# Performance work log

Hardware: AMD Instinct MI355X
Metric: run time of the kernel (lower is better)

The kernel has to match this reference:

```python
import jax, jax.numpy as jnp
import numpy as np

H, W, WIN = 16, 6, 3  # tile height/width, SSIM window
C1, C2 = 0.01 ** 2, 0.03 ** 2  # kornia ssim constants (max_val=1.0)


def _gauss_kernel3():
    # kornia get_gaussian_kernel2d((3,3),(1.5,1.5)), normalized
    c = jnp.arange(WIN, dtype=jnp.float32) - (WIN - 1) / 2.0
    g = jnp.exp(-(c ** 2) / (2.0 * 1.5 ** 2))
    g = g / g.sum()
    k2 = jnp.outer(g, g)
    return (k2 / k2.sum()).reshape(-1)  # (9,)


def _patches3(x):
    # x: (N,H,W) -> (N,H,W,9) 3x3 reflect-padded neighborhoods (kornia filter2d border 'reflect')
    xp = jnp.pad(x, ((0, 0), (1, 1), (1, 1)), mode='reflect')
    rows = [xp[:, i:i + H, j:j + W] for i in range(WIN) for j in range(WIN)]
    return jnp.stack(rows, axis=-1)


def setup_inputs() -> dict:
    key = jax.random.key(0)
    k1, k2 = jax.random.split(key)
    img_tensor = jax.random.uniform(k1, (1, 1, 1024, 768), dtype=jnp.float32)
    chars = jax.random.uniform(k2, (95, 1, 16, 6), dtype=jnp.float32)
    return {"img_tensor": img_tensor, "chars": chars}


def reference(img_tensor, chars):
    img_h, img_w = img_tensor.shape[-2], img_tensor.shape[-1]
    n_rows, n_cols = img_h // H, img_w // W
    # nn.Unfold(kernel=(H,W), stride=(H,W)): row-major tiles, each flattened (h,w)
    tiles = img_tensor[0, 0].reshape(n_rows, H, n_cols, W).transpose(0, 2, 1, 3)
    tiles = tiles.reshape(-1, H, W)              # (nt,H,W)
    refs = chars[:, 0]                           # (nr,H,W)

    kflat = _gauss_kernel3()                     # (9,)
    Tp = _patches3(tiles)                        # (nt,H,W,9)
    Rp = _patches3(refs)                         # (nr,H,W,9)

    # per-image windowed stats (computed ONCE per tile / per ref)
    mu_t = Tp @ kflat                            # (nt,H,W)
    mu_r = Rp @ kflat                            # (nr,H,W)
    ex2_t = (Tp ** 2) @ kflat
    ex2_r = (Rp ** 2) @ kflat
    sig_t = ex2_t - mu_t ** 2
    sig_r = ex2_r - mu_r ** 2

    # pairwise cross term E[t*r]: contract kernel over the 3x3 window axis
    exr = jnp.einsum('thwk,rhwk->trhw', Tp * kflat, Rp)  # (nt,nr,H,W)

    mt = mu_t[:, None]                           # (nt,1,H,W)
    mr = mu_r[None, :]                           # (1,nr,H,W)
    sig_tr = exr - mt * mr
    num = (2.0 * mt * mr + C1) * (2.0 * sig_tr + C2)
    den = (mt ** 2 + mr ** 2 + C1) * (sig_t[:, None] + sig_r[None, :] + C2)
    scores = (num / den).mean(axis=(2, 3))       # (nt,nr)

    dens_t = tiles.mean(axis=(1, 2))             # (nt,)
    dens_r = refs.mean(axis=(1, 2))              # (nr,)
    scores = scores - 3.0 * jnp.abs(dens_t[:, None] - dens_r[None, :])

    best_indices = jnp.argmax(scores, axis=1)
    return best_indices.reshape(-1, n_cols)
```

## Files before the change

### kernel.cpp

```cpp
#include <hip/hip_runtime.h>
#include <math.h>


static constexpr float kC1 = 1.0e-4f;
static constexpr float kC2 = 9.0e-4f;

struct KF { float k[9]; };

__device__ __forceinline__ int refl(int x, int n) {
  if (x < 0) return -x;
  if (x >= n) return 2 * n - 2 - x;
  return x;
}

__global__ __launch_bounds__(128) void refprep_kernel(
    const float* __restrict__ chars, float* __restrict__ refdata,
    float* __restrict__ densR, KF kf) {
  const int hw = blockIdx.x;
  const int r = threadIdx.x;
  if (r >= 96) return;
  const int rp = r / 6 + 16 * (r % 6);
  float* row = refdata + ((size_t)hw * 96 + rp) * 12;
  const int h = hw / 6, w = hw % 6;
  if (r < 95) {
    const float* cb = chars + r * 96;
    float mu = 0.f, ex2 = 0.f;
    float wrv[9];
#pragma unroll
    for (int i = 0; i < 3; ++i) {
      const int hh = refl(h + i - 1, 16);
#pragma unroll
      for (int j = 0; j < 3; ++j) {
        const int ww = refl(w + j - 1, 6);
        const float p = cb[hh * 6 + ww];
        const float kv = kf.k[i * 3 + j];
        wrv[i * 3 + j] = 2.0f * kv * p;
        mu += kv * p;
        ex2 += kv * p * p;
      }
    }
    const float sig = ex2 - mu * mu;
#pragma unroll
    for (int k = 0; k < 9; ++k) row[k] = wrv[k];
    row[9]  = 2.0f * mu;
    row[10] = mu * mu + kC1;
    row[11] = sig + kC2;
  } else {
#pragma unroll
    for (int k = 0; k < 9; ++k) row[k] = 0.f;
    row[9]  = 0.f;
    row[10] = kC1;
    row[11] = kC2;
  }
  if (hw == 0) {
    if (r < 95) {
      float s = 0.f;
      for (int i = 0; i < 96; ++i) s += chars[r * 96 + i];
      densR[r] = s * (1.0f / 96.0f);
    } else {
      densR[r] = 0.f;
    }
  }
}

__device__ __forceinline__ void stage_px(const float* __restrict__ src,
                                         float* dst, int lane) {
  const uintptr_t gs = (uintptr_t)src;
  const uintptr_t ls = (uintptr_t)dst;
#define G_(off) ((const __attribute__((address_space(1))) void*)(gs + (off)))
#define L_(off) ((__attribute__((address_space(3))) void*)(uint32_t)(ls + (off)))
  __builtin_amdgcn_global_load_lds(G_(0    + lane * 16), L_(0),    16, 0, 0);
  __builtin_amdgcn_global_load_lds(G_(1024 + lane * 16), L_(1024), 16, 0, 0);
  __builtin_amdgcn_global_load_lds(G_(2048 + lane * 16), L_(2048), 16, 0, 0);
  __builtin_amdgcn_global_load_lds(G_(3072 + lane * 16), L_(3072), 16, 0, 0);
  __builtin_amdgcn_global_load_lds(G_(4096 + lane * 4),  L_(4096), 4, 0, 0);
  __builtin_amdgcn_global_load_lds(G_(4352 + lane * 4),  L_(4352), 4, 0, 0);
#undef G_
#undef L_
}

__global__ __launch_bounds__(512, 2)
void ssim_main_kernel(
    const float* __restrict__ img, const float* __restrict__ refdata,
    const float* __restrict__ densR, int* __restrict__ out, KF kf) {
  __shared__ float smem[29184];
  __shared__ float densT[32];
  float* padT = smem;
  float* statT = smem + 4608;

  const int tid = threadIdx.x;
  const int w = tid >> 6;
  const int lane = tid & 63;
  const int tthr = lane >> 4;
  const int rthr = lane & 15;
  const int tl0 = tthr * 8;
  const int blk = blockIdx.x;
  const int row0 = blk >> 2;
  const int c0 = (blk & 3) * 32;
  const int hwBase = w * 12;
  float* rbuf = smem + 10752 + w * 2304;

  stage_px(refdata + (size_t)hwBase * 1152, rbuf, lane);

  for (int idx = tid; idx < 4608; idx += 512) {
    const int c = idx >> 5, tl = idx & 31;
    const int ph = c >> 3, pw = c & 7;
    const int h = refl(ph - 1, 16), ww = refl(pw - 1, 6);
    padT[idx] = img[(row0 * 16 + h) * 768 + (c0 + tl) * 6 + ww];
  }
  __syncthreads();

  if (tid < 32) {
    float s = 0.f;
    for (int h = 0; h < 16; ++h)
      for (int ww = 0; ww < 6; ++ww)
        s += padT[((h + 1) * 8 + (ww + 1)) * 32 + tid];
    densT[tid] = s * (1.0f / 96.0f);
  }
  for (int idx = tid; idx < 3072; idx += 512) {
    const int hw = idx >> 5, tl = idx & 31;
    const int h = hw / 6, ww = hw % 6;
    float mu = 0.f, ex2 = 0.f;
#pragma unroll
    for (int i = 0; i < 3; ++i)
#pragma unroll
      for (int j = 0; j < 3; ++j) {
        const float p = padT[((h + i) * 8 + (ww + j)) * 32 + tl];
        const float kv = kf.k[i * 3 + j];
        mu += kv * p;
        ex2 += kv * p * p;
      }
    statT[idx] = mu;
    statT[3072 + idx] = ex2 - mu * mu;
  }
  __syncthreads();

  float score[8][6];
#pragma unroll
  for (int i = 0; i < 8; ++i)
#pragma unroll
    for (int j = 0; j < 6; ++j) score[i][j] = 0.f;

  int pb = (2 * w) * 8 * 32 + tl0;
  int sbase = hwBase * 32 + tl0;
  const float* refsrc = refdata + (size_t)(hwBase + 1) * 1152;
  int w6 = 0;

#pragma unroll 1
  for (int it = 0; it < 12; ++it) {
    const float* buf = rbuf + (it & 1) * 1152;

    if (it < 11) {
      stage_px(refsrc, rbuf + ((it + 1) & 1) * 1152, lane);
      asm volatile("s_waitcnt vmcnt(6)" ::: "memory");
    } else {
      asm volatile("s_waitcnt vmcnt(0)" ::: "memory");
    }
    refsrc += 1152;

    float tp[9][8];
#pragma unroll
    for (int ik = 0; ik < 3; ++ik)
#pragma unroll
      for (int jk = 0; jk < 3; ++jk) {
        const int k = ik * 3 + jk;
        const float4 a = *(const float4*)&padT[pb + (ik * 8 + jk) * 32];
        const float4 b = *(const float4*)&padT[pb + (ik * 8 + jk) * 32 + 4];
        tp[k][0] = a.x; tp[k][1] = a.y; tp[k][2] = a.z; tp[k][3] = a.w;
        tp[k][4] = b.x; tp[k][5] = b.y; tp[k][6] = b.z; tp[k][7] = b.w;
      }

    float mu[8], sg[8], mt2[8];
    {
      float4 v;
      v = *(const float4*)&statT[sbase];            mu[0]=v.x; mu[1]=v.y; mu[2]=v.z; mu[3]=v.w;
      v = *(const float4*)&statT[sbase + 4];        mu[4]=v.x; mu[5]=v.y; mu[6]=v.z; mu[7]=v.w;
      v = *(const float4*)&statT[3072 + sbase];     sg[0]=v.x; sg[1]=v.y; sg[2]=v.z; sg[3]=v.w;
      v = *(const float4*)&statT[3072 + sbase + 4]; sg[4]=v.x; sg[5]=v.y; sg[6]=v.z; sg[7]=v.w;
#pragma unroll
      for (int i = 0; i < 8; ++i) mt2[i] = mu[i] * mu[i];
    }

#pragma unroll
    for (int j = 0; j < 6; ++j) {
      const int rb = (rthr + 16 * j) * 12;
      const float4 wa = *(const float4*)&buf[rb];
      const float4 wb = *(const float4*)&buf[rb + 4];
      const float4 wc = *(const float4*)&buf[rb + 8];
#pragma unroll
      for (int i = 0; i < 8; ++i) {
        float ev = fmaf(tp[0][i], wa.x, kC2);
        ev = fmaf(tp[1][i], wa.y, ev);
        ev = fmaf(tp[2][i], wa.z, ev);
        ev = fmaf(tp[3][i], wa.w, ev);
        ev = fmaf(tp[4][i], wb.x, ev);
        ev = fmaf(tp[5][i], wb.y, ev);
        ev = fmaf(tp[6][i], wb.z, ev);
        ev = fmaf(tp[7][i], wb.w, ev);
        ev = fmaf(tp[8][i], wc.x, ev);
        const float am = mu[i] * wc.y;
        const float n1 = am + kC1;
        const float n2 = ev - am;
        const float d1 = mt2[i] + wc.z;
        const float d2 = sg[i] + wc.w;
        const float nn = n1 * n2;
        const float dd = d1 * d2;
        const float r0v = __builtin_amdgcn_rcpf(dd);
        const float r1v = r0v * fmaf(-dd, r0v, 2.0f);
        score[i][j] = fmaf(nn, r1v, score[i][j]);
      }
    }

    pb += (w6 == 5) ? 96 : 32;
    w6 = (w6 == 5) ? 0 : w6 + 1;
    sbase += 32;
  }

  __syncthreads();
  float* sb = smem;
#pragma unroll
  for (int i = 0; i < 8; ++i)
#pragma unroll
    for (int j = 0; j < 6; ++j)
      sb[w * 3104 + (tl0 + i) * 97 + (rthr * 6 + j)] = score[i][j];
  __syncthreads();

  {
    const int tile = tid >> 4, rt = tid & 15;
    const float dt = densT[tile];
    float best = -1e30f; int bi = 0;
#pragma unroll
    for (int q = 0; q < 6; ++q) {
      const int r = rt * 6 + q;
      if (r < 95) {
        float s = 0.f;
#pragma unroll
        for (int g = 0; g < 8; ++g) s += sb[g * 3104 + tile * 97 + r];
        s = s * (1.0f / 96.0f) - 3.0f * fabsf(dt - densR[r]);
        if (s > best) { best = s; bi = r; }
      }
    }
#pragma unroll
    for (int m = 8; m >= 1; m >>= 1) {
      const float ob = __shfl_xor(best, m, 64);
      const int oi = __shfl_xor(bi, m, 64);
      if (ob > best || (ob == best && oi < bi)) { best = ob; bi = oi; }
    }
    if (rt == 0) out[row0 * 128 + c0 + tile] = bi;
  }
}

extern "C" void kernel_launch(void* const* d_in, const int* in_sizes, int n_in,
                              void* d_out, int out_size, void* d_ws, size_t ws_size,
                              hipStream_t stream) {
  (void)in_sizes; (void)n_in; (void)out_size; (void)ws_size;
  const float* img = (const float*)d_in[0];
  const float* chars = (const float*)d_in[1];
  int* out = (int*)d_out;
  float* refdata = (float*)d_ws;
  float* densR = refdata + 110592;

  KF kf;
  {
    float gg[3], s = 0.f;
    for (int i = 0; i < 3; ++i) {
      const float c = (float)i - 1.0f;
      gg[i] = expf(-(c * c) / (2.0f * 1.5f * 1.5f));
      s += gg[i];
    }
    float gn[3];
    for (int i = 0; i < 3; ++i) gn[i] = gg[i] / s;
    float k2[9]; float ks = 0.f;
    for (int i = 0; i < 3; ++i)
      for (int j = 0; j < 3; ++j) { k2[i * 3 + j] = gn[i] * gn[j]; ks += k2[i * 3 + j]; }
    for (int k = 0; k < 9; ++k) kf.k[k] = k2[k] / ks;
  }

  hipLaunchKernelGGL(refprep_kernel, dim3(96), dim3(128), 0, stream,
                     chars, refdata, densR, kf);
  hipLaunchKernelGGL(ssim_main_kernel, dim3(256), dim3(512), 0, stream,
                     img, refdata, densR, out, kf);
}
```

Baseline: 50.38 us.

## Pair warps to share reference staging and halve per-thread tile work

Warps are grouped in pairs. Each pair covers 24 window positions instead of each warp covering 12, and each warp handles 4 tiles per thread instead of 8. The two warps of a pair each stage half of the reference buffer, which cuts total LDS from about 29K floats to about 20K and reduces per-thread registers. The aim is more occupancy and less staging traffic. In exchange the loop runs twice as many iterations and adds a block-wide __syncthreads every iteration to hand off the double buffer. The Newton refinement of the reciprocal is also dropped, which slightly lowers precision and could in principle flip near-tie argmax results.

```diff
diff --git a/kernel.cpp b/kernel.cpp
--- a/kernel.cpp
+++ b/kernel.cpp
@@ -63,18 +63,15 @@
   }
 }
 
-__device__ __forceinline__ void stage_px(const float* __restrict__ src,
-                                         float* dst, int lane) {
-  const uintptr_t gs = (uintptr_t)src;
-  const uintptr_t ls = (uintptr_t)dst;
+__device__ __forceinline__ void stage_half(const float* __restrict__ src,
+                                           float* dst, int lane, int half) {
+  const uintptr_t gs = (uintptr_t)src + half * 2304;
+  const uintptr_t ls = (uintptr_t)dst + half * 2304;
 #define G_(off) ((const __attribute__((address_space(1))) void*)(gs + (off)))
 #define L_(off) ((__attribute__((address_space(3))) void*)(uint32_t)(ls + (off)))
   __builtin_amdgcn_global_load_lds(G_(0    + lane * 16), L_(0),    16, 0, 0);
   __builtin_amdgcn_global_load_lds(G_(1024 + lane * 16), L_(1024), 16, 0, 0);
-  __builtin_amdgcn_global_load_lds(G_(2048 + lane * 16), L_(2048), 16, 0, 0);
-  __builtin_amdgcn_global_load_lds(G_(3072 + lane * 16), L_(3072), 16, 0, 0);
-  __builtin_amdgcn_global_load_lds(G_(4096 + lane * 4),  L_(4096), 4, 0, 0);
-  __builtin_amdgcn_global_load_lds(G_(4352 + lane * 4),  L_(4352), 4, 0, 0);
+  __builtin_amdgcn_global_load_lds(G_(2048 + lane * 4),  L_(2048), 4, 0, 0);
 #undef G_
 #undef L_
 }
@@ -83,24 +80,26 @@
 void ssim_main_kernel(
     const float* __restrict__ img, const float* __restrict__ refdata,
     const float* __restrict__ densR, int* __restrict__ out, KF kf) {
-  __shared__ float smem[29184];
+  __shared__ float smem[19968];
   __shared__ float densT[32];
   float* padT = smem;
   float* statT = smem + 4608;
 
   const int tid = threadIdx.x;
   const int w = tid >> 6;
+  const int p = w >> 1;
+  const int half = w & 1;
   const int lane = tid & 63;
   const int tthr = lane >> 4;
   const int rthr = lane & 15;
-  const int tl0 = tthr * 8;
+  const int tl0 = half * 16 + tthr * 4;
   const int blk = blockIdx.x;
   const int row0 = blk >> 2;
   const int c0 = (blk & 3) * 32;
-  const int hwBase = w * 12;
-  float* rbuf = smem + 10752 + w * 2304;
-
-  stage_px(refdata + (size_t)hwBase * 1152, rbuf, lane);
+  const int hwBase = p * 24;
+  float* pairbuf = smem + 10752 + p * 2304;
+
+  stage_half(refdata + (size_t)hwBase * 1152, pairbuf, lane, half);
 
   for (int idx = tid; idx < 4608; idx += 512) {
     const int c = idx >> 5, tl = idx & 31;
@@ -125,60 +124,55 @@
     for (int i = 0; i < 3; ++i)
 #pragma unroll
       for (int j = 0; j < 3; ++j) {
-        const float p = padT[((h + i) * 8 + (ww + j)) * 32 + tl];
+        const float p2 = padT[((h + i) * 8 + (ww + j)) * 32 + tl];
         const float kv = kf.k[i * 3 + j];
-        mu += kv * p;
-        ex2 += kv * p * p;
+        mu += kv * p2;
+        ex2 += kv * p2 * p2;
       }
     statT[idx] = mu;
     statT[3072 + idx] = ex2 - mu * mu;
   }
   __syncthreads();
 
-  float score[8][6];
-#pragma unroll
-  for (int i = 0; i < 8; ++i)
+  float score[4][6];
+#pragma unroll
+  for (int i = 0; i < 4; ++i)
 #pragma unroll
     for (int j = 0; j < 6; ++j) score[i][j] = 0.f;
 
-  int pb = (2 * w) * 8 * 32 + tl0;
+  int w6 = 0;
+  int pb = (hwBase / 6) * 256 + tl0;
   int sbase = hwBase * 32 + tl0;
   const float* refsrc = refdata + (size_t)(hwBase + 1) * 1152;
-  int w6 = 0;
+  int slot = 0;
 
 #pragma unroll 1
-  for (int it = 0; it < 12; ++it) {
-    const float* buf = rbuf + (it & 1) * 1152;
-
-    if (it < 11) {
-      stage_px(refsrc, rbuf + ((it + 1) & 1) * 1152, lane);
-      asm volatile("s_waitcnt vmcnt(6)" ::: "memory");
-    } else {
-      asm volatile("s_waitcnt vmcnt(0)" ::: "memory");
-    }
-    refsrc += 1152;
-
-    float tp[9][8];
+  for (int it = 0; it < 24; ++it) {
+    const float* buf = pairbuf + slot * 1152;
+
+    if (it < 23) {
+      stage_half(refsrc, pairbuf + (slot ^ 1) * 1152, lane, half);
+      refsrc += 1152;
+    }
+
+    float tp[9][4];
 #pragma unroll
     for (int ik = 0; ik < 3; ++ik)
 #pragma unroll
       for (int jk = 0; jk < 3; ++jk) {
         const int k = ik * 3 + jk;
         const float4 a = *(const float4*)&padT[pb + (ik * 8 + jk) * 32];
-        const float4 b = *(const float4*)&padT[pb + (ik * 8 + jk) * 32 + 4];
         tp[k][0] = a.x; tp[k][1] = a.y; tp[k][2] = a.z; tp[k][3] = a.w;
-        tp[k][4] = b.x; tp[k][5] = b.y; tp[k][6] = b.z; tp[k][7] = b.w;
-      }
-
-    float mu[8], sg[8], mt2[8];
+      }
+
+    float mu[4], sg[4], mt2[4];
     {
-      float4 v;
-      v = *(const float4*)&statT[sbase];            mu[0]=v.x; mu[1]=v.y; mu[2]=v.z; mu[3]=v.w;
-      v = *(const float4*)&statT[sbase + 4];        mu[4]=v.x; mu[5]=v.y; mu[6]=v.z; mu[7]=v.w;
-      v = *(const float4*)&statT[3072 + sbase];     sg[0]=v.x; sg[1]=v.y; sg[2]=v.z; sg[3]=v.w;
-      v = *(const float4*)&statT[3072 + sbase + 4]; sg[4]=v.x; sg[5]=v.y; sg[6]=v.z; sg[7]=v.w;
-#pragma unroll
-      for (int i = 0; i < 8; ++i) mt2[i] = mu[i] * mu[i];
+      const float4 m = *(const float4*)&statT[sbase];
+      const float4 s = *(const float4*)&statT[3072 + sbase];
+      mu[0]=m.x; mu[1]=m.y; mu[2]=m.z; mu[3]=m.w;
+      sg[0]=s.x; sg[1]=s.y; sg[2]=s.z; sg[3]=s.w;
+#pragma unroll
+      for (int i = 0; i < 4; ++i) mt2[i] = mu[i] * mu[i];
     }
 
 #pragma unroll
@@ -188,7 +182,7 @@
       const float4 wb = *(const float4*)&buf[rb + 4];
       const float4 wc = *(const float4*)&buf[rb + 8];
 #pragma unroll
-      for (int i = 0; i < 8; ++i) {
+      for (int i = 0; i < 4; ++i) {
         float ev = fmaf(tp[0][i], wa.x, kC2);
         ev = fmaf(tp[1][i], wa.y, ev);
         ev = fmaf(tp[2][i], wa.z, ev);
@@ -206,23 +200,24 @@
         const float nn = n1 * n2;
         const float dd = d1 * d2;
         const float r0v = __builtin_amdgcn_rcpf(dd);
-        const float r1v = r0v * fmaf(-dd, r0v, 2.0f);
-        score[i][j] = fmaf(nn, r1v, score[i][j]);
-      }
-    }
+        score[i][j] = fmaf(nn, r0v, score[i][j]);
+      }
+    }
+
+    __syncthreads();
 
     pb += (w6 == 5) ? 96 : 32;
     w6 = (w6 == 5) ? 0 : w6 + 1;
     sbase += 32;
-  }
-
-  __syncthreads();
+    slot ^= 1;
+  }
+
   float* sb = smem;
 #pragma unroll
-  for (int i = 0; i < 8; ++i)
+  for (int i = 0; i < 4; ++i)
 #pragma unroll
     for (int j = 0; j < 6; ++j)
-      sb[w * 3104 + (tl0 + i) * 97 + (rthr * 6 + j)] = score[i][j];
+      sb[p * 3104 + (tl0 + i) * 97 + (rthr * 6 + j)] = score[i][j];
   __syncthreads();
 
   {
@@ -235,7 +230,7 @@
       if (r < 95) {
         float s = 0.f;
 #pragma unroll
-        for (int g = 0; g < 8; ++g) s += sb[g * 3104 + tile * 97 + r];
+        for (int g = 0; g < 4; ++g) s += sb[g * 3104 + tile * 97 + r];
         s = s * (1.0f / 96.0f) - 3.0f * fabsf(dt - densR[r]);
         if (s > best) { best = s; bi = r; }
       }
```

Result: slower. 60.91 us (+20.9%).

## Split SSIM work across tile-row halves with a separate combine kernel

Applied to the files above, without the earlier changes.

Each 32-tile block is split into two blocks, each covering half the tile rows (48 of 96 pixel positions), so the grid doubles to 512 blocks of 384 threads. Partial score sums and densities go to workspace and a new combine kernel reduces them and does the argmax. It also drops the Newton refinement step after the reciprocal, which loosens accuracy and could flip argmax ties. The change adds one launch plus global-memory partial traffic, and keeps the old single-kernel path as a fallback when the workspace is too small.

```diff
diff --git a/kernel.cpp b/kernel.cpp
--- a/kernel.cpp
+++ b/kernel.cpp
@@ -79,14 +79,13 @@
 #undef L_
 }
 
-__global__ __launch_bounds__(512, 2)
-void ssim_main_kernel(
+__global__ __launch_bounds__(384, 2)
+void ssim_half_kernel(
     const float* __restrict__ img, const float* __restrict__ refdata,
-    const float* __restrict__ densR, int* __restrict__ out, KF kf) {
-  __shared__ float smem[29184];
-  __shared__ float densT[32];
+    float* __restrict__ part, float* __restrict__ densP, KF kf) {
+  __shared__ float smem[19456];
   float* padT = smem;
-  float* statT = smem + 4608;
+  float* statT = smem + 2560;
 
   const int tid = threadIdx.x;
   const int w = tid >> 6;
@@ -95,43 +94,47 @@
   const int rthr = lane & 15;
   const int tl0 = tthr * 8;
   const int blk = blockIdx.x;
-  const int row0 = blk >> 2;
-  const int c0 = (blk & 3) * 32;
-  const int hwBase = w * 12;
-  float* rbuf = smem + 10752 + w * 2304;
+  const int row0 = blk >> 3;
+  const int colg = (blk >> 1) & 3;
+  const int half = blk & 1;
+  const int c0 = colg * 32;
+  const int bxy = row0 * 4 + colg;
+  const int trb = half * 8;
+  const int hwBase = half * 48 + w * 8;
+  float* rbuf = smem + 5632 + w * 2304;
 
   stage_px(refdata + (size_t)hwBase * 1152, rbuf, lane);
 
-  for (int idx = tid; idx < 4608; idx += 512) {
+  for (int idx = tid; idx < 2560; idx += 384) {
     const int c = idx >> 5, tl = idx & 31;
-    const int ph = c >> 3, pw = c & 7;
-    const int h = refl(ph - 1, 16), ww = refl(pw - 1, 6);
+    const int pr = c >> 3, pw = c & 7;
+    const int h = refl(trb + pr - 1, 16), ww = refl(pw - 1, 6);
     padT[idx] = img[(row0 * 16 + h) * 768 + (c0 + tl) * 6 + ww];
   }
   __syncthreads();
 
   if (tid < 32) {
     float s = 0.f;
-    for (int h = 0; h < 16; ++h)
-      for (int ww = 0; ww < 6; ++ww)
-        s += padT[((h + 1) * 8 + (ww + 1)) * 32 + tid];
-    densT[tid] = s * (1.0f / 96.0f);
-  }
-  for (int idx = tid; idx < 3072; idx += 512) {
-    const int hw = idx >> 5, tl = idx & 31;
-    const int h = hw / 6, ww = hw % 6;
+    for (int pr = 1; pr <= 8; ++pr)
+      for (int pw = 1; pw <= 6; ++pw)
+        s += padT[(pr * 8 + pw) * 32 + tid];
+    densP[half * 8192 + row0 * 128 + c0 + tid] = s;
+  }
+  for (int idx = tid; idx < 1536; idx += 384) {
+    const int hwl = idx >> 5, tl = idx & 31;
+    const int hl = hwl / 6, w6l = hwl % 6;
     float mu = 0.f, ex2 = 0.f;
 #pragma unroll
     for (int i = 0; i < 3; ++i)
 #pragma unroll
       for (int j = 0; j < 3; ++j) {
-        const float p = padT[((h + i) * 8 + (ww + j)) * 32 + tl];
+        const float p = padT[((hl + i) * 8 + (w6l + j)) * 32 + tl];
         const float kv = kf.k[i * 3 + j];
         mu += kv * p;
         ex2 += kv * p * p;
       }
     statT[idx] = mu;
-    statT[3072 + idx] = ex2 - mu * mu;
+    statT[1536 + idx] = ex2 - mu * mu;
   }
   __syncthreads();
 
@@ -141,16 +144,16 @@
 #pragma unroll
     for (int j = 0; j < 6; ++j) score[i][j] = 0.f;
 
-  int pb = (2 * w) * 8 * 32 + tl0;
-  int sbase = hwBase * 32 + tl0;
+  int w6 = (w * 8) % 6;
+  int pb = ((w * 8) / 6 * 8 + w6) * 32 + tl0;
+  int sbase = (w * 8) * 32 + tl0;
   const float* refsrc = refdata + (size_t)(hwBase + 1) * 1152;
-  int w6 = 0;
 
 #pragma unroll 1
-  for (int it = 0; it < 12; ++it) {
+  for (int it = 0; it < 8; ++it) {
     const float* buf = rbuf + (it & 1) * 1152;
 
-    if (it < 11) {
+    if (it < 7) {
       stage_px(refsrc, rbuf + ((it + 1) & 1) * 1152, lane);
       asm volatile("s_waitcnt vmcnt(6)" ::: "memory");
     } else {
@@ -175,8 +178,8 @@
       float4 v;
       v = *(const float4*)&statT[sbase];            mu[0]=v.x; mu[1]=v.y; mu[2]=v.z; mu[3]=v.w;
       v = *(const float4*)&statT[sbase + 4];        mu[4]=v.x; mu[5]=v.y; mu[6]=v.z; mu[7]=v.w;
-      v = *(const float4*)&statT[3072 + sbase];     sg[0]=v.x; sg[1]=v.y; sg[2]=v.z; sg[3]=v.w;
-      v = *(const float4*)&statT[3072 + sbase + 4]; sg[4]=v.x; sg[5]=v.y; sg[6]=v.z; sg[7]=v.w;
+      v = *(const float4*)&statT[1536 + sbase];     sg[0]=v.x; sg[1]=v.y; sg[2]=v.z; sg[3]=v.w;
+      v = *(const float4*)&statT[1536 + sbase + 4]; sg[4]=v.x; sg[5]=v.y; sg[6]=v.z; sg[7]=v.w;
 #pragma unroll
       for (int i = 0; i < 8; ++i) mt2[i] = mu[i] * mu[i];
     }
@@ -206,11 +209,210 @@
         const float nn = n1 * n2;
         const float dd = d1 * d2;
         const float r0v = __builtin_amdgcn_rcpf(dd);
-        const float r1v = r0v * fmaf(-dd, r0v, 2.0f);
-        score[i][j] = fmaf(nn, r1v, score[i][j]);
-      }
-    }
-
+        score[i][j] = fmaf(nn, r0v, score[i][j]);
+      }
+    }
+
+    pb += (w6 == 5) ? 96 : 32;
+    w6 = (w6 == 5) ? 0 : w6 + 1;
+    sbase += 32;
+  }
+
+  __syncthreads();
+  float* sb = smem;
+#pragma unroll
+  for (int i = 0; i < 8; ++i)
+#pragma unroll
+    for (int j = 0; j < 6; ++j)
+      sb[w * 3104 + (tl0 + i) * 97 + (rthr * 6 + j)] = score[i][j];
+  __syncthreads();
+
+  {
+    const int r = tid >> 2;
+    const int tq = tid & 3;
+    float* dst = part + (((size_t)(half * 256 + bxy) * 96 + r) * 32 + tq * 8);
+#pragma unroll
+    for (int t = 0; t < 8; ++t) {
+      const int tile = tq * 8 + t;
+      float s = 0.f;
+#pragma unroll
+      for (int g = 0; g < 6; ++g) s += sb[g * 3104 + tile * 97 + r];
+      dst[t] = s;
+    }
+  }
+}
+
+__global__ __launch_bounds__(512) void combine_kernel(
+    const float* __restrict__ part, const float* __restrict__ densP,
+    const float* __restrict__ densR, int* __restrict__ out) {
+  __shared__ float sb2[32 * 97];
+  __shared__ float sdens[32];
+  const int tid = threadIdx.x;
+  const int bxy = blockIdx.x;
+  const float* p0 = part + (size_t)bxy * 3072;
+  const float* p1 = part + (size_t)(256 + bxy) * 3072;
+
+  for (int idx = tid; idx < 3072; idx += 512) {
+    const int r = idx >> 5, t = idx & 31;
+    sb2[t * 97 + r] = p0[idx] + p1[idx];
+  }
+  if (tid < 32) {
+    const int g = (bxy >> 2) * 128 + (bxy & 3) * 32 + tid;
+    sdens[tid] = (densP[g] + densP[8192 + g]) * (1.0f / 96.0f);
+  }
+  __syncthreads();
+
+  const int tile = tid >> 4, rt = tid & 15;
+  const float dt = sdens[tile];
+  float best = -1e30f; int bi = 0;
+#pragma unroll
+  for (int q = 0; q < 6; ++q) {
+    const int r = rt * 6 + q;
+    if (r < 95) {
+      float s = sb2[tile * 97 + r] * (1.0f / 96.0f)
+              - 3.0f * fabsf(dt - densR[r]);
+      if (s > best) { best = s; bi = r; }
+    }
+  }
+#pragma unroll
+  for (int m = 8; m >= 1; m >>= 1) {
+    const float ob = __shfl_xor(best, m, 64);
+    const int oi = __shfl_xor(bi, m, 64);
+    if (ob > best || (ob == best && oi < bi)) { best = ob; bi = oi; }
+  }
+  if (rt == 0) {
+    const int g = (bxy >> 2) * 128 + (bxy & 3) * 32 + tile;
+    out[g] = bi;
+  }
+}
+
+__global__ __launch_bounds__(512, 2)
+void ssim_full_kernel(
+    const float* __restrict__ img, const float* __restrict__ refdata,
+    const float* __restrict__ densR, int* __restrict__ out, KF kf) {
+  __shared__ float smem[29184];
+  __shared__ float densT[32];
+  float* padT = smem;
+  float* statT = smem + 4608;
+
+  const int tid = threadIdx.x;
+  const int w = tid >> 6;
+  const int lane = tid & 63;
+  const int tthr = lane >> 4;
+  const int rthr = lane & 15;
+  const int tl0 = tthr * 8;
+  const int blk = blockIdx.x;
+  const int row0 = blk >> 2;
+  const int c0 = (blk & 3) * 32;
+  const int hwBase = w * 12;
+  float* rbuf = smem + 10752 + w * 2304;
+
+  stage_px(refdata + (size_t)hwBase * 1152, rbuf, lane);
+
+  for (int idx = tid; idx < 4608; idx += 512) {
+    const int c = idx >> 5, tl = idx & 31;
+    const int ph = c >> 3, pw = c & 7;
+    const int h = refl(ph - 1, 16), ww = refl(pw - 1, 6);
+    padT[idx] = img[(row0 * 16 + h) * 768 + (c0 + tl) * 6 + ww];
+  }
+  __syncthreads();
+
+  if (tid < 32) {
+    float s = 0.f;
+    for (int h = 0; h < 16; ++h)
+      for (int ww = 0; ww < 6; ++ww)
+        s += padT[((h + 1) * 8 + (ww + 1)) * 32 + tid];
+    densT[tid] = s * (1.0f / 96.0f);
+  }
+  for (int idx = tid; idx < 3072; idx += 512) {
+    const int hw = idx >> 5, tl = idx & 31;
+    const int h = hw / 6, ww = hw % 6;
+    float mu = 0.f, ex2 = 0.f;
+#pragma unroll
+    for (int i = 0; i < 3; ++i)
+#pragma unroll
+      for (int j = 0; j < 3; ++j) {
+        const float p = padT[((h + i) * 8 + (ww + j)) * 32 + tl];
+        const float kv = kf.k[i * 3 + j];
+        mu += kv * p;
+        ex2 += kv * p * p;
+      }
+    statT[idx] = mu;
+    statT[3072 + idx] = ex2 - mu * mu;
+  }
+  __syncthreads();
+
+  float score[8][6];
+#pragma unroll
+  for (int i = 0; i < 8; ++i)
+#pragma unroll
+    for (int j = 0; j < 6; ++j) score[i][j] = 0.f;
+
+  int w6 = 0;
+  int pb = (2 * w) * 8 * 32 + tl0;
+  int sbase = hwBase * 32 + tl0;
+  const float* refsrc = refdata + (size_t)(hwBase + 1) * 1152;
+
+#pragma unroll 1
+  for (int it = 0; it < 12; ++it) {
+    const float* buf = rbuf + (it & 1) * 1152;
+    if (it < 11) {
+      stage_px(refsrc, rbuf + ((it + 1) & 1) * 1152, lane);
+      asm volatile("s_waitcnt vmcnt(6)" ::: "memory");
+    } else {
+      asm volatile("s_waitcnt vmcnt(0)" ::: "memory");
+    }
+    refsrc += 1152;
+
+    float tp[9][8];
+#pragma unroll
+    for (int ik = 0; ik < 3; ++ik)
+#pragma unroll
+      for (int jk = 0; jk < 3; ++jk) {
+        const int k = ik * 3 + jk;
+        const float4 a = *(const float4*)&padT[pb + (ik * 8 + jk) * 32];
+        const float4 b = *(const float4*)&padT[pb + (ik * 8 + jk) * 32 + 4];
+        tp[k][0] = a.x; tp[k][1] = a.y; tp[k][2] = a.z; tp[k][3] = a.w;
+        tp[k][4] = b.x; tp[k][5] = b.y; tp[k][6] = b.z; tp[k][7] = b.w;
+      }
+    float mu[8], sg[8], mt2[8];
+    {
+      float4 v;
+      v = *(const float4*)&statT[sbase];            mu[0]=v.x; mu[1]=v.y; mu[2]=v.z; mu[3]=v.w;
+      v = *(const float4*)&statT[sbase + 4];        mu[4]=v.x; mu[5]=v.y; mu[6]=v.z; mu[7]=v.w;
+      v = *(const float4*)&statT[3072 + sbase];     sg[0]=v.x; sg[1]=v.y; sg[2]=v.z; sg[3]=v.w;
+      v = *(const float4*)&statT[3072 + sbase + 4]; sg[4]=v.x; sg[5]=v.y; sg[6]=v.z; sg[7]=v.w;
+#pragma unroll
+      for (int i = 0; i < 8; ++i) mt2[i] = mu[i] * mu[i];
+    }
+#pragma unroll
+    for (int j = 0; j < 6; ++j) {
+      const int rb = (rthr + 16 * j) * 12;
+      const float4 wa = *(const float4*)&buf[rb];
+      const float4 wb = *(const float4*)&buf[rb + 4];
+      const float4 wc = *(const float4*)&buf[rb + 8];
+#pragma unroll
+      for (int i = 0; i < 8; ++i) {
+        float ev = fmaf(tp[0][i], wa.x, kC2);
+        ev = fmaf(tp[1][i], wa.y, ev);
+        ev = fmaf(tp[2][i], wa.z, ev);
+        ev = fmaf(tp[3][i], wa.w, ev);
+        ev = fmaf(tp[4][i], wb.x, ev);
+        ev = fmaf(tp[5][i], wb.y, ev);
+        ev = fmaf(tp[6][i], wb.z, ev);
+        ev = fmaf(tp[7][i], wb.w, ev);
+        ev = fmaf(tp[8][i], wc.x, ev);
+        const float am = mu[i] * wc.y;
+        const float n1 = am + kC1;
+        const float n2 = ev - am;
+        const float d1 = mt2[i] + wc.z;
+        const float d2 = sg[i] + wc.w;
+        const float nn = n1 * n2;
+        const float dd = d1 * d2;
+        const float r0v = __builtin_amdgcn_rcpf(dd);
+        score[i][j] = fmaf(nn, r0v, score[i][j]);
+      }
+    }
     pb += (w6 == 5) ? 96 : 32;
     w6 = (w6 == 5) ? 0 : w6 + 1;
     sbase += 32;
@@ -253,12 +455,15 @@
 extern "C" void kernel_launch(void* const* d_in, const int* in_sizes, int n_in,
                               void* d_out, int out_size, void* d_ws, size_t ws_size,
                               hipStream_t stream) {
-  (void)in_sizes; (void)n_in; (void)out_size; (void)ws_size;
+  (void)in_sizes; (void)n_in; (void)out_size;
   const float* img = (const float*)d_in[0];
   const float* chars = (const float*)d_in[1];
   int* out = (int*)d_out;
   float* refdata = (float*)d_ws;
   float* densR = refdata + 110592;
+  float* part = refdata + 110688;
+  float* densP = part + 1572864;
+  const size_t need_bytes = (size_t)(110688 + 1572864 + 16384) * 4;
 
   KF kf;
   {
@@ -278,6 +483,13 @@
 
   hipLaunchKernelGGL(refprep_kernel, dim3(96), dim3(128), 0, stream,
                      chars, refdata, densR, kf);
-  hipLaunchKernelGGL(ssim_main_kernel, dim3(256), dim3(512), 0, stream,
-                     img, refdata, densR, out, kf);
-}
+  if (ws_size >= need_bytes) {
+    hipLaunchKernelGGL(ssim_half_kernel, dim3(512), dim3(384), 0, stream,
+                       img, refdata, part, densP, kf);
+    hipLaunchKernelGGL(combine_kernel, dim3(256), dim3(512), 0, stream,
+                       part, densP, densR, out);
+  } else {
+    hipLaunchKernelGGL(ssim_full_kernel, dim3(256), dim3(512), 0, stream,
+                       img, refdata, densR, out, kf);
+  }
+}
```

Result: slower. 66.46 us (+31.9%).

## Split SSIM over pixel quarters with register-resident refs and a combine kernel

Applied to the files above, without the earlier changes.

Adds a new main path that splits each tile's pixels into four row-quarters across blocks, doubling the grid. Each thread handles one tile and twelve refs, reading ref coefficients straight from global/L1 instead of staging them through LDS with async copies. Partial scores are written to a workspace, and a second kernel sums them, applies the density penalty and takes the argmax. The reciprocal Newton refinement is also dropped, which trades accuracy for fewer instructions and could flip near-tie argmax results. The cost is an extra kernel launch and about 12 MB of partial-score traffic through global memory.

```diff
diff --git a/kernel.cpp b/kernel.cpp
--- a/kernel.cpp
+++ b/kernel.cpp
@@ -19,8 +19,7 @@
   const int hw = blockIdx.x;
   const int r = threadIdx.x;
   if (r >= 96) return;
-  const int rp = r / 6 + 16 * (r % 6);
-  float* row = refdata + ((size_t)hw * 96 + rp) * 12;
+  float* row = refdata + ((size_t)hw * 96 + r) * 12;
   const int h = hw / 6, w = hw % 6;
   if (r < 95) {
     const float* cb = chars + r * 96;
@@ -61,6 +60,159 @@
       densR[r] = 0.f;
     }
   }
+}
+
+__global__ __launch_bounds__(512, 2)
+void ssim_reg_kernel(
+    const float* __restrict__ img, const float* __restrict__ refdata,
+    float* __restrict__ part, float* __restrict__ densP, KF kf) {
+  __shared__ float padT[3072];
+  __shared__ float statT[3072];
+
+  const int tid = threadIdx.x;
+  const int lane = tid & 63;
+  const int w = tid >> 6;
+  const int blk = blockIdx.x;
+  const int q = blk & 3;
+  const int b2 = blk >> 2;
+  const int row0 = b2 >> 1;
+  const int ch = b2 & 1;
+
+  for (int idx = tid; idx < 3072; idx += 512) {
+    const int c = idx >> 6, tl = idx & 63;
+    const int pr = c >> 3, pc = c & 7;
+    const int h = refl(q * 4 + pr - 1, 16), ww = refl(pc - 1, 6);
+    padT[idx] = img[(row0 * 16 + h) * 768 + ch * 384 + tl * 6 + ww];
+  }
+  __syncthreads();
+
+  if (tid < 64) {
+    float s = 0.f;
+    for (int pr = 1; pr <= 4; ++pr)
+      for (int pc = 1; pc <= 6; ++pc)
+        s += padT[(pr * 8 + pc) * 64 + tid];
+    densP[q * 8192 + row0 * 128 + ch * 64 + tid] = s;
+  }
+  for (int idx = tid; idx < 1536; idx += 512) {
+    const int hwl = idx >> 6, tl = idx & 63;
+    const int hl = hwl / 6, wl = hwl - hl * 6;
+    float mu = 0.f, ex2 = 0.f;
+#pragma unroll
+    for (int i = 0; i < 3; ++i)
+#pragma unroll
+      for (int j = 0; j < 3; ++j) {
+        const float p = padT[((hl + i) * 8 + (wl + j)) * 64 + tl];
+        const float kv = kf.k[i * 3 + j];
+        mu += kv * p;
+        ex2 += kv * p * p;
+      }
+    statT[idx] = mu;
+    statT[1536 + idx] = ex2 - mu * mu;
+  }
+  __syncthreads();
+
+  float score[12];
+#pragma unroll
+  for (int j = 0; j < 12; ++j) score[j] = 0.f;
+
+  int tapoff = lane;
+  int statoff = lane;
+  int c6 = 0;
+  const float* refpx = refdata + (size_t)(q * 24) * 1152 + w * 12 * 12;
+
+#pragma unroll 1
+  for (int p = 0; p < 24; ++p) {
+    float t0 = padT[tapoff];
+    float t1 = padT[tapoff + 64];
+    float t2 = padT[tapoff + 128];
+    float t3 = padT[tapoff + 512];
+    float t4 = padT[tapoff + 576];
+    float t5 = padT[tapoff + 640];
+    float t6 = padT[tapoff + 1024];
+    float t7 = padT[tapoff + 1088];
+    float t8 = padT[tapoff + 1152];
+    const float mu = statT[statoff];
+    const float sg = statT[1536 + statoff];
+    const float mt2 = mu * mu;
+
+#pragma unroll
+    for (int j = 0; j < 12; ++j) {
+      const float* rw = refpx + j * 12;
+      const float4 wa = *(const float4*)(rw);
+      const float4 wb = *(const float4*)(rw + 4);
+      const float4 wc = *(const float4*)(rw + 8);
+      float ev = fmaf(t0, wa.x, kC2);
+      ev = fmaf(t1, wa.y, ev);
+      ev = fmaf(t2, wa.z, ev);
+      ev = fmaf(t3, wa.w, ev);
+      ev = fmaf(t4, wb.x, ev);
+      ev = fmaf(t5, wb.y, ev);
+      ev = fmaf(t6, wb.z, ev);
+      ev = fmaf(t7, wb.w, ev);
+      ev = fmaf(t8, wc.x, ev);
+      const float am = mu * wc.y;
+      const float n1 = am + kC1;
+      const float n2 = ev - am;
+      const float d1 = mt2 + wc.z;
+      const float d2 = sg + wc.w;
+      const float r0v = __builtin_amdgcn_rcpf(d1 * d2);
+      score[j] = fmaf(n1 * n2, r0v, score[j]);
+    }
+
+    tapoff += (c6 == 5) ? 192 : 64;
+    c6 = (c6 == 5) ? 0 : c6 + 1;
+    statoff += 64;
+    refpx += 1152;
+  }
+
+  float* dst = part + ((size_t)q * 128 + b2) * 6144 + (w * 12) * 64 + lane;
+#pragma unroll
+  for (int j = 0; j < 12; ++j) dst[j * 64] = score[j];
+}
+
+__global__ __launch_bounds__(512) void combine4_kernel(
+    const float* __restrict__ part, const float* __restrict__ densP,
+    const float* __restrict__ densR, int* __restrict__ out) {
+  __shared__ float sb2[64 * 97];
+  __shared__ float sdens[64];
+  const int tid = threadIdx.x;
+  const int b2 = blockIdx.x;
+
+  for (int idx = tid; idx < 6144; idx += 512) {
+    const int r = idx >> 6, t = idx & 63;
+    const float s = part[(size_t)(0 * 128 + b2) * 6144 + idx]
+                  + part[(size_t)(1 * 128 + b2) * 6144 + idx]
+                  + part[(size_t)(2 * 128 + b2) * 6144 + idx]
+                  + part[(size_t)(3 * 128 + b2) * 6144 + idx];
+    sb2[t * 97 + r] = s;
+  }
+  if (tid < 64) {
+    const int gt = (b2 >> 1) * 128 + (b2 & 1) * 64 + tid;
+    sdens[tid] = (densP[gt] + densP[8192 + gt] + densP[16384 + gt]
+                  + densP[24576 + gt]) * (1.0f / 96.0f);
+  }
+  __syncthreads();
+
+  const int tile = tid >> 3, rt = tid & 7;
+  const float dt = sdens[tile];
+  float best = -1e30f; int bi = 0;
+#pragma unroll
+  for (int qq = 0; qq < 12; ++qq) {
+    const int r = rt * 12 + qq;
+    if (r < 95) {
+      const float s = sb2[tile * 97 + r] * (1.0f / 96.0f)
+                    - 3.0f * fabsf(dt - densR[r]);
+      if (s > best) { best = s; bi = r; }
+    }
+  }
+#pragma unroll
+  for (int m = 4; m >= 1; m >>= 1) {
+    const float ob = __shfl_xor(best, m, 64);
+    const int oi = __shfl_xor(bi, m, 64);
+    if (ob > best || (ob == best && oi < bi)) { best = ob; bi = oi; }
+  }
+  if (rt == 0)
+    out[(b2 >> 1) * 128 + (b2 & 1) * 64 + tile] = bi;
 }
 
 __device__ __forceinline__ void stage_px(const float* __restrict__ src,
@@ -80,7 +232,7 @@
 }
 
 __global__ __launch_bounds__(512, 2)
-void ssim_main_kernel(
+void ssim_full_kernel(
     const float* __restrict__ img, const float* __restrict__ refdata,
     const float* __restrict__ densR, int* __restrict__ out, KF kf) {
   __shared__ float smem[29184];
@@ -141,15 +293,14 @@
 #pragma unroll
     for (int j = 0; j < 6; ++j) score[i][j] = 0.f;
 
+  int w6 = 0;
   int pb = (2 * w) * 8 * 32 + tl0;
   int sbase = hwBase * 32 + tl0;
   const float* refsrc = refdata + (size_t)(hwBase + 1) * 1152;
-  int w6 = 0;
 
 #pragma unroll 1
   for (int it = 0; it < 12; ++it) {
     const float* buf = rbuf + (it & 1) * 1152;
-
     if (it < 11) {
       stage_px(refsrc, rbuf + ((it + 1) & 1) * 1152, lane);
       asm volatile("s_waitcnt vmcnt(6)" ::: "memory");
@@ -169,7 +320,6 @@
         tp[k][0] = a.x; tp[k][1] = a.y; tp[k][2] = a.z; tp[k][3] = a.w;
         tp[k][4] = b.x; tp[k][5] = b.y; tp[k][6] = b.z; tp[k][7] = b.w;
       }
-
     float mu[8], sg[8], mt2[8];
     {
       float4 v;
@@ -180,7 +330,6 @@
 #pragma unroll
       for (int i = 0; i < 8; ++i) mt2[i] = mu[i] * mu[i];
     }
-
 #pragma unroll
     for (int j = 0; j < 6; ++j) {
       const int rb = (rthr + 16 * j) * 12;
@@ -203,14 +352,10 @@
         const float n2 = ev - am;
         const float d1 = mt2[i] + wc.z;
         const float d2 = sg[i] + wc.w;
-        const float nn = n1 * n2;
-        const float dd = d1 * d2;
-        const float r0v = __builtin_amdgcn_rcpf(dd);
-        const float r1v = r0v * fmaf(-dd, r0v, 2.0f);
-        score[i][j] = fmaf(nn, r1v, score[i][j]);
-      }
-    }
-
+        const float r0v = __builtin_amdgcn_rcpf(d1 * d2);
+        score[i][j] = fmaf(n1 * n2, r0v, score[i][j]);
+      }
+    }
     pb += (w6 == 5) ? 96 : 32;
     w6 = (w6 == 5) ? 0 : w6 + 1;
     sbase += 32;
@@ -222,7 +367,7 @@
   for (int i = 0; i < 8; ++i)
 #pragma unroll
     for (int j = 0; j < 6; ++j)
-      sb[w * 3104 + (tl0 + i) * 97 + (rthr * 6 + j)] = score[i][j];
+      sb[w * 3104 + (tl0 + i) * 97 + (rthr + 16 * j)] = score[i][j];
   __syncthreads();
 
   {
@@ -230,8 +375,8 @@
     const float dt = densT[tile];
     float best = -1e30f; int bi = 0;
 #pragma unroll
-    for (int q = 0; q < 6; ++q) {
-      const int r = rt * 6 + q;
+    for (int qq = 0; qq < 6; ++qq) {
+      const int r = rt * 6 + qq;
       if (r < 95) {
         float s = 0.f;
 #pragma unroll
@@ -253,12 +398,15 @@
 extern "C" void kernel_launch(void* const* d_in, const int* in_sizes, int n_in,
                               void* d_out, int out_size, void* d_ws, size_t ws_size,
                               hipStream_t stream) {
-  (void)in_sizes; (void)n_in; (void)out_size; (void)ws_size;
+  (void)in_sizes; (void)n_in; (void)out_size;
   const float* img = (const float*)d_in[0];
   const float* chars = (const float*)d_in[1];
   int* out = (int*)d_out;
   float* refdata = (float*)d_ws;
   float* densR = refdata + 110592;
+  float* part = refdata + 110688;
+  float* densP = part + 3145728;
+  const size_t need_bytes = (size_t)(110688 + 3145728 + 32768) * 4;
 
   KF kf;
   {
@@ -278,6 +426,13 @@
 
   hipLaunchKernelGGL(refprep_kernel, dim3(96), dim3(128), 0, stream,
                      chars, refdata, densR, kf);
-  hipLaunchKernelGGL(ssim_main_kernel, dim3(256), dim3(512), 0, stream,
-                     img, refdata, densR, out, kf);
-}
+  if (ws_size >= need_bytes) {
+    hipLaunchKernelGGL(ssim_reg_kernel, dim3(512), dim3(512), 0, stream,
+                       img, refdata, part, densP, kf);
+    hipLaunchKernelGGL(combine4_kernel, dim3(128), dim3(512), 0, stream,
+                       part, densP, densR, out);
+  } else {
+    hipLaunchKernelGGL(ssim_full_kernel, dim3(256), dim3(512), 0, stream,
+                       img, refdata, densR, out, kf);
+  }
+}
```

Measured after the change: 122.1 us. 2.42x slower.
